# Performance work log

Measured on AMD Instinct MI355X. Metric: run time of the kernel, lower is better.

## Reference

```python
import jax, jax.numpy as jnp
import numpy as np
from jax import lax

EPS = 1e-8
ROOT_2 = 1.41421
STYLE_SIZE = 512
OUT_CH = 512
STYLE_SCALE = (2.0 / STYLE_SIZE) ** 0.5   # Weight_Scaling(style_size): equalized-LR sqrt(2/fan_in)
OUT_SCALE = (2.0 / (OUT_CH * 1 * 1)) ** 0.5  # Weight_Scaling(out_channels*1*1)


def setup_inputs() -> dict:
    key = jax.random.key(0)
    ks = jax.random.split(key, 10)
    B, Cin, Cout, H, S = 8, 512, 512, 32, 512
    return {
        "x": jax.random.normal(ks[0], (B, Cin, H, H), dtype=jnp.float32),
        "style_base": jax.random.normal(ks[1], (B, S), dtype=jnp.float32),
        "noise": jax.random.normal(ks[2], (B, 1, 2 * H, 2 * H), dtype=jnp.float32),
        "t": jax.random.normal(ks[3], (B, Cout, 2 * H, 2 * H), dtype=jnp.float32),
        # learned params
        "affine_w": jax.random.normal(ks[4], (Cin, S), dtype=jnp.float32) * (1.0 / np.sqrt(S)),
        "affine_b": jnp.zeros((Cin,), dtype=jnp.float32),
        "conv_w": jax.random.normal(ks[5], (Cout, Cin, 3, 3), dtype=jnp.float32),
        "conv_b": jnp.zeros((1, Cout, 1, 1), dtype=jnp.float32),
        "prelu_a": jnp.asarray(0.25, dtype=jnp.float32),
        "noise_scalar": jnp.zeros((1, Cout, 1, 1), dtype=jnp.float32) + 0.1,
        "out_w": jax.random.normal(ks[6], (3, Cout, 1, 1), dtype=jnp.float32) * (1.0 / np.sqrt(Cout)),
        "out_b": jnp.zeros((3,), dtype=jnp.float32),
    }


def reference(x, style_base, noise, t, affine_w, affine_b, conv_w, conv_b,
              prelu_a, noise_scalar, out_w, out_b):
    B, Cin, H, W = x.shape
    # style_std = affine(Weight_Scaling(style_base)) + 1  -> [B, Cin]
    style_std = (style_base * STYLE_SCALE) @ affine_w.T + affine_b + 1.0

    # bilinear x2 upsample (align_corners=False == half-pixel, matches jax.image.resize)
    x = jax.image.resize(x, (B, Cin, 2 * H, 2 * W), method="bilinear")

    # modulated conv with L2 demodulation, expressed as input-scale + conv + output-scale
    # per-sample weight w_b[o,i,k,l] = w[o,i,k,l]*s[b,i] / ||w*s||_b,o
    wsq = jnp.sum(conv_w ** 2, axis=(2, 3))                      # [O, I]
    demod = 1.0 / jnp.sqrt(jnp.einsum("oi,bi->bo", wsq, style_std ** 2) + EPS)  # [B, O]
    xm = x * style_std[:, :, None, None]
    y = lax.conv_general_dilated(xm, conv_w, (1, 1), "SAME",
                                 dimension_numbers=("NCHW", "OIHW", "NCHW"))
    y = y * demod[:, :, None, None] + conv_b + noise_scalar * noise
    # PReLU (single shared slope)
    y = jnp.where(y >= 0, y, prelu_a * y)

    # out branch: skip add, scale, toRGB 1x1 conv, clamp
    y = (y + t) / ROOT_2
    out = lax.conv_general_dilated(y * OUT_SCALE, out_w, (1, 1), "SAME",
                                   dimension_numbers=("NCHW", "OIHW", "NCHW"))
    out = jnp.clip(out + out_b[None, :, None, None], 0.0, 1.0)
    return (y, out)
```

## Files before the change

### kernel.cpp

```cpp
#include <hip/hip_runtime.h>


typedef short bf16x8 __attribute__((ext_vector_type(8)));
typedef short short8v __attribute__((ext_vector_type(8)));
typedef float f32x16 __attribute__((ext_vector_type(16)));

#define WS_STYLE 0
#define WS_DEMOD 16384
#define WS_WSQ   32768
#define WS_WPACK 1081344
#define WS_XM    5799936

__device__ __forceinline__ short f2bf(float f) {
  unsigned u = __float_as_uint(f);
  u += 0x7FFFu + ((u >> 16) & 1u);
  return (short)(u >> 16);
}

__device__ __forceinline__ void gld16(const short* g, char* l) {
  __builtin_amdgcn_global_load_lds((const __attribute__((address_space(1))) void*)g,
                                   (__attribute__((address_space(3))) void*)l,
                                   16, 0, 0);
}

__global__ void k_style(const float* __restrict__ sb, const float* __restrict__ aw,
                        const float* __restrict__ ab, float* __restrict__ style) {
  __shared__ float s_sb[512];
  int b = blockIdx.x;
  for (int i = threadIdx.x; i < 512; i += 256) s_sb[i] = sb[b * 512 + i] * 0.0625f;
  __syncthreads();
  for (int i = threadIdx.x; i < 512; i += 256) {
    const float4* wrow = (const float4*)(aw + (size_t)i * 512);
    float acc = 0.f;
    #pragma unroll 4
    for (int s4 = 0; s4 < 128; ++s4) {
      float4 w4 = wrow[s4];
      float4 sv = *(const float4*)(s_sb + s4 * 4);
      acc += w4.x * sv.x + w4.y * sv.y + w4.z * sv.z + w4.w * sv.w;
    }
    style[b * 512 + i] = acc + ab[i] + 1.0f;
  }
}

__global__ void k_wsq(const float* __restrict__ cw, float* __restrict__ wsq) {
  int idx = blockIdx.x * 256 + threadIdx.x;
  const float* p = cw + (size_t)idx * 9;
  float s = 0.f;
  #pragma unroll
  for (int j = 0; j < 9; ++j) s += p[j] * p[j];
  wsq[idx] = s;
}

__global__ void k_demod(const float* __restrict__ wsq, const float* __restrict__ style,
                        float* __restrict__ demod) {
  int wid = threadIdx.x >> 6, lane = threadIdx.x & 63;
  int idx = blockIdx.x * 4 + wid;
  int b = idx >> 9, o = idx & 511;
  const float* wr = wsq + (size_t)o * 512;
  const float* ss = style + b * 512;
  float sum = 0.f;
  #pragma unroll
  for (int k = 0; k < 8; ++k) {
    int i = k * 64 + lane;
    float s = ss[i];
    sum += wr[i] * s * s;
  }
  #pragma unroll
  for (int off = 32; off; off >>= 1) sum += __shfl_down(sum, off);
  if (lane == 0) demod[b * 512 + o] = rsqrtf(sum + 1e-8f);
}

__global__ void k_upsample(const float* __restrict__ x, const float* __restrict__ style,
                           short* __restrict__ xm) {
  int b = blockIdx.x / 66, hp = blockIdx.x % 66;
  short* xmp = xm + ((size_t)b * 66 + hp) * 66 * 512;
  if (hp == 0 || hp == 65) {
    short8v z = {0, 0, 0, 0, 0, 0, 0, 0};
    for (int u = threadIdx.x; u < 66 * 512 / 8; u += 256) ((short8v*)xmp)[u] = z;
    return;
  }
  int h = hp - 1;
  int j0 = (h >> 1) - 1 + (h & 1);
  float fj = (h & 1) ? 0.25f : 0.75f;
  int j0c = j0 < 0 ? 0 : j0;
  int j1c = j0 + 1 > 31 ? 31 : j0 + 1;
  __shared__ float xt[2][64][33];
  int ccc = threadIdx.x & 63;
  int wsub = threadIdx.x >> 6;
  for (int c0 = 0; c0 < 512; c0 += 64) {
    __syncthreads();
    #pragma unroll 4
    for (int k = 0; k < 16; ++k) {
      int idx = k * 256 + threadIdx.x;
      int ii = idx & 31, cc = (idx >> 5) & 63, jj = idx >> 11;
      xt[jj][cc][ii] = x[(((size_t)b * 512 + c0 + cc) * 32 + (jj ? j1c : j0c)) * 32 + ii];
    }
    __syncthreads();
    float sstyle = style[b * 512 + c0 + ccc];
    #pragma unroll 4
    for (int wk = 0; wk < 16; ++wk) {
      int w = wk * 4 + wsub;
      int i0 = (w >> 1) - 1 + (w & 1);
      float fi = (w & 1) ? 0.25f : 0.75f;
      int i0c = i0 < 0 ? 0 : i0;
      int i1c = i0 + 1 > 31 ? 31 : i0 + 1;
      float v0 = xt[0][ccc][i0c] * (1.f - fi) + xt[0][ccc][i1c] * fi;
      float v1 = xt[1][ccc][i0c] * (1.f - fi) + xt[1][ccc][i1c] * fi;
      float v = (v0 * (1.f - fj) + v1 * fj) * sstyle;
      xmp[(size_t)(w + 1) * 512 + c0 + ccc] = f2bf(v);
    }
    if (wsub == 0) {
      xmp[c0 + ccc] = 0;
      xmp[(size_t)65 * 512 + c0 + ccc] = 0;
    }
  }
}

__global__ void k_packw(const float* __restrict__ cw, short* __restrict__ wpk) {
  int unit = blockIdx.x * 256 + threadIdx.x;
  int s = unit >> 11;
  int rem = unit & 2047;
  int o = rem >> 2, sp = rem & 3;
  int tap = s >> 4, cc = s & 15;
  int i0 = cc * 32 + ((sp ^ (o & 3)) << 3);
  const float* src = cw + ((size_t)o * 512 + i0) * 9 + tap;
  short8v v;
  #pragma unroll
  for (int j = 0; j < 8; ++j) v[j] = f2bf(src[j * 9]);
  *(short8v*)(wpk + (size_t)unit * 8) = v;
}

__global__ __launch_bounds__(512, 2) void k_conv(
    const short* __restrict__ xm, const short* __restrict__ wpk,
    const float* __restrict__ demod, const float* __restrict__ convb,
    const float* __restrict__ nscal, const float* __restrict__ noise,
    const float* __restrict__ t, const float* __restrict__ prelu_a,
    float* __restrict__ y) {
  __shared__ char XMs[2][25344];
  __shared__ char WTs[2][16384];

  int tid = threadIdx.x;
  int bid = blockIdx.x;
  int nt = bid & 1, sp_t = bid >> 1;
  int b = sp_t >> 4, hq = sp_t & 15;
  int wid = tid >> 6, lane = tid & 63;
  int wo = wid & 1, wsrow = wid >> 1;
  int l31 = lane & 31, lg = lane >> 5;

  const short* xb = xm + ((size_t)b * 66 + hq * 4) * 66 * 512;
  int wb0 = ((wo * 128 + l31) << 6) + ((lg ^ (l31 & 3)) << 4);

  #pragma unroll
  for (int k = 0; k < 3; ++k) {
    int u = k * 512 + tid;
    int r = u / 264, rem = u - r * 264;
    int wp = rem >> 2, spp = rem & 3;
    gld16(xb + (size_t)(r * 66 + wp) * 512 + ((spp ^ (wp & 3)) << 3), XMs[0] + u * 16);
  }
  if (tid < 48) {
    int u = 1536 + tid;
    int rem = u - 1320;
    int wp = rem >> 2, spp = rem & 3;
    gld16(xb + (size_t)(5 * 66 + wp) * 512 + ((spp ^ (wp & 3)) << 3), XMs[0] + u * 16);
  }
  {
    const short* wsrc = wpk + (size_t)(nt * 256) * 32;
    gld16(wsrc + tid * 8, WTs[0] + tid * 16);
    gld16(wsrc + (512 + tid) * 8, WTs[0] + (512 + tid) * 16);
  }

  f32x16 zf = {0,0,0,0,0,0,0,0,0,0,0,0,0,0,0,0};
  f32x16 acc[4][2];
  #pragma unroll
  for (int i = 0; i < 4; ++i) { acc[i][0] = zf; acc[i][1] = zf; }

  __syncthreads();

  #pragma unroll 1
  for (int cc = 0; cc < 16; ++cc) {
    const char* XMc = XMs[cc & 1];
    char* XMn = XMs[(cc & 1) ^ 1];
    int pw = cc & 1;
    #pragma unroll
    for (int tap = 0; tap < 9; ++tap) {
      const int kh = tap / 3, kw = tap % 3;
      const char* WTc = WTs[(pw + tap) & 1];
      char* WTn = (char*)WTs[(pw + tap + 1) & 1];

      if (!(cc == 15 && tap == 8)) {
        int ntap = (tap < 8) ? (tap + 1) : 0;
        int ncc  = (tap < 8) ? cc : (cc + 1);
        const short* wsrc = wpk + ((size_t)((ntap * 16 + ncc) * 512) + nt * 256) * 32;
        gld16(wsrc + tid * 8, WTn + tid * 16);
        gld16(wsrc + (512 + tid) * 8, WTn + (512 + tid) * 16);
      }
      if (tap >= 3 && cc < 15) {
        const int r = tap - 3;
        if (tid < 264) {
          int wp = tid >> 2, spp = tid & 3;
          gld16(xb + (size_t)(r * 66 + wp) * 512 + (cc + 1) * 32 + ((spp ^ (wp & 3)) << 3),
                XMn + (r * 264 + tid) * 16);
        }
      }

      int a = l31 + kw;
      int xo = ((wsrow + kh) * 66 + a) * 64 + ((lg ^ (a & 3)) << 4);
      bf16x8 xf00 = *(const bf16x8*)(XMc + xo);
      bf16x8 xf01 = *(const bf16x8*)(XMc + xo + 2048);
      bf16x8 xf10 = *(const bf16x8*)(XMc + (xo ^ 32));
      bf16x8 xf11 = *(const bf16x8*)(XMc + ((xo ^ 32) + 2048));
      bf16x8 wf00 = *(const bf16x8*)(WTc + wb0);
      bf16x8 wf01 = *(const bf16x8*)(WTc + wb0 + 2048);
      bf16x8 wf02 = *(const bf16x8*)(WTc + wb0 + 4096);
      bf16x8 wf03 = *(const bf16x8*)(WTc + wb0 + 6144);
      bf16x8 wf10 = *(const bf16x8*)(WTc + (wb0 ^ 32));
      bf16x8 wf11 = *(const bf16x8*)(WTc + ((wb0 ^ 32) + 2048));
      bf16x8 wf12 = *(const bf16x8*)(WTc + ((wb0 ^ 32) + 4096));
      bf16x8 wf13 = *(const bf16x8*)(WTc + ((wb0 ^ 32) + 6144));

      acc[0][0] = __builtin_amdgcn_mfma_f32_32x32x16_bf16(wf00, xf00, acc[0][0], 0, 0, 0);
      acc[0][1] = __builtin_amdgcn_mfma_f32_32x32x16_bf16(wf00, xf01, acc[0][1], 0, 0, 0);
      acc[1][0] = __builtin_amdgcn_mfma_f32_32x32x16_bf16(wf01, xf00, acc[1][0], 0, 0, 0);
      acc[1][1] = __builtin_amdgcn_mfma_f32_32x32x16_bf16(wf01, xf01, acc[1][1], 0, 0, 0);
      acc[2][0] = __builtin_amdgcn_mfma_f32_32x32x16_bf16(wf02, xf00, acc[2][0], 0, 0, 0);
      acc[2][1] = __builtin_amdgcn_mfma_f32_32x32x16_bf16(wf02, xf01, acc[2][1], 0, 0, 0);
      acc[3][0] = __builtin_amdgcn_mfma_f32_32x32x16_bf16(wf03, xf00, acc[3][0], 0, 0, 0);
      acc[3][1] = __builtin_amdgcn_mfma_f32_32x32x16_bf16(wf03, xf01, acc[3][1], 0, 0, 0);
      acc[0][0] = __builtin_amdgcn_mfma_f32_32x32x16_bf16(wf10, xf10, acc[0][0], 0, 0, 0);
      acc[0][1] = __builtin_amdgcn_mfma_f32_32x32x16_bf16(wf10, xf11, acc[0][1], 0, 0, 0);
      acc[1][0] = __builtin_amdgcn_mfma_f32_32x32x16_bf16(wf11, xf10, acc[1][0], 0, 0, 0);
      acc[1][1] = __builtin_amdgcn_mfma_f32_32x32x16_bf16(wf11, xf11, acc[1][1], 0, 0, 0);
      acc[2][0] = __builtin_amdgcn_mfma_f32_32x32x16_bf16(wf12, xf10, acc[2][0], 0, 0, 0);
      acc[2][1] = __builtin_amdgcn_mfma_f32_32x32x16_bf16(wf12, xf11, acc[2][1], 0, 0, 0);
      acc[3][0] = __builtin_amdgcn_mfma_f32_32x32x16_bf16(wf13, xf10, acc[3][0], 0, 0, 0);
      acc[3][1] = __builtin_amdgcn_mfma_f32_32x32x16_bf16(wf13, xf11, acc[3][1], 0, 0, 0);

      __syncthreads();
    }
  }

  float pa = prelu_a[0];
  const float inv_r2 = 1.0f / 1.41421f;
  int h = hq * 4 + wsrow;
  float nz0 = noise[((size_t)b * 64 + h) * 64 + l31];
  float nz1 = noise[((size_t)b * 64 + h) * 64 + 32 + l31];
  #pragma unroll
  for (int cf = 0; cf < 4; ++cf) {
    #pragma unroll
    for (int reg = 0; reg < 16; ++reg) {
      int orow = (reg & 3) + 8 * (reg >> 2) + 4 * lg;
      int o = nt * 256 + wo * 128 + cf * 32 + orow;
      float dm = demod[b * 512 + o];
      float cb = convb[o];
      float ns = nscal[o];
      #pragma unroll
      for (int nf = 0; nf < 2; ++nf) {
        int w = nf * 32 + l31;
        float v = acc[cf][nf][reg];
        v = v * dm + cb + ns * (nf ? nz1 : nz0);
        v = (v >= 0.f) ? v : pa * v;
        size_t oi = (((size_t)b * 512 + o) * 64 + h) * 64 + w;
        v = (v + t[oi]) * inv_r2;
        y[oi] = v;
      }
    }
  }
}

__global__ void k_rgb(const float* __restrict__ y, const float* __restrict__ ow,
                      const float* __restrict__ ob, float* __restrict__ out) {
  int b = blockIdx.x >> 6, h = blockIdx.x & 63;
  int w = threadIdx.x & 63, g = threadIdx.x >> 6;
  const float* yb = y + (((size_t)b * 512) * 64 + h) * 64 + w;
  float s0 = 0.f, s1 = 0.f, s2 = 0.f;
  for (int o = g * 128; o < g * 128 + 128; ++o) {
    float v = yb[(size_t)o * 4096];
    s0 += v * ow[o];
    s1 += v * ow[512 + o];
    s2 += v * ow[1024 + o];
  }
  __shared__ float red[3][4][64];
  red[0][g][w] = s0; red[1][g][w] = s1; red[2][g][w] = s2;
  __syncthreads();
  if (threadIdx.x < 192) {
    int c = threadIdx.x >> 6, ww = threadIdx.x & 63;
    float s = red[c][0][ww] + red[c][1][ww] + red[c][2][ww] + red[c][3][ww];
    s = s * 0.0625f + ob[c];
    s = fminf(fmaxf(s, 0.f), 1.f);
    out[(((size_t)b * 3 + c) * 64 + h) * 64 + ww] = s;
  }
}

extern "C" void kernel_launch(void* const* d_in, const int* in_sizes, int n_in,
                              void* d_out, int out_size, void* d_ws, size_t ws_size,
                              hipStream_t stream) {
  const float* x     = (const float*)d_in[0];
  const float* sb    = (const float*)d_in[1];
  const float* noise = (const float*)d_in[2];
  const float* t     = (const float*)d_in[3];
  const float* aw    = (const float*)d_in[4];
  const float* ab    = (const float*)d_in[5];
  const float* cw    = (const float*)d_in[6];
  const float* cb    = (const float*)d_in[7];
  const float* pa    = (const float*)d_in[8];
  const float* ns    = (const float*)d_in[9];
  const float* ow    = (const float*)d_in[10];
  const float* ob    = (const float*)d_in[11];
  char* ws = (char*)d_ws;
  float* style = (float*)(ws + WS_STYLE);
  float* demod = (float*)(ws + WS_DEMOD);
  float* wsq   = (float*)(ws + WS_WSQ);
  short* wpk   = (short*)(ws + WS_WPACK);
  short* xm    = (short*)(ws + WS_XM);
  float* y   = (float*)d_out;
  float* out = y + 16777216;

  k_style<<<8, 256, 0, stream>>>(sb, aw, ab, style);
  k_wsq<<<1024, 256, 0, stream>>>(cw, wsq);
  k_demod<<<1024, 256, 0, stream>>>(wsq, style, demod);
  k_upsample<<<528, 256, 0, stream>>>(x, style, xm);
  k_packw<<<1152, 256, 0, stream>>>(cw, wpk);
  k_conv<<<256, 512, 0, stream>>>(xm, wpk, demod, cb, ns, noise, t, pa, y);
  k_rgb<<<512, 256, 0, stream>>>(y, ow, ob, out);
}
```

Before: 269.9 us.

## Halve conv spatial tile to 2 rows, 256 threads, new LDS swizzle, MFMA priority

The conv kernel now computes 2 output rows per block with 4 waves instead of 4 rows with 8 waves, doubling the grid to 512 blocks. The aim is better CU occupancy and load balance across the many compute units. The LDS XOR swizzle changes from (idx&3) to ((idx>>1)&3), applied consistently in weight packing and activation loads, to reduce bank conflicts. The activation prefetch is spread over taps 0-5, and s_setprio raises wave priority around the MFMA block. In exchange, each weight tile is reused over half as many pixels, so weight traffic from L2 per FLOP doubles.

Result: faster. 254.2 us (-5.8%).

```diff
diff --git a/kernel.cpp b/kernel.cpp
--- a/kernel.cpp
+++ b/kernel.cpp
@@ -122,7 +122,7 @@
   int rem = unit & 2047;
   int o = rem >> 2, sp = rem & 3;
   int tap = s >> 4, cc = s & 15;
-  int i0 = cc * 32 + ((sp ^ (o & 3)) << 3);
+  int i0 = cc * 32 + ((sp ^ ((o >> 1) & 3)) << 3);
   const float* src = cw + ((size_t)o * 512 + i0) * 9 + tap;
   short8v v;
   #pragma unroll
@@ -130,43 +130,42 @@
   *(short8v*)(wpk + (size_t)unit * 8) = v;
 }
 
-__global__ __launch_bounds__(512, 2) void k_conv(
+__global__ __launch_bounds__(256, 2) void k_conv(
     const short* __restrict__ xm, const short* __restrict__ wpk,
     const float* __restrict__ demod, const float* __restrict__ convb,
     const float* __restrict__ nscal, const float* __restrict__ noise,
     const float* __restrict__ t, const float* __restrict__ prelu_a,
     float* __restrict__ y) {
-  __shared__ char XMs[2][25344];
+  __shared__ char XMs[2][16896];
   __shared__ char WTs[2][16384];
 
   int tid = threadIdx.x;
   int bid = blockIdx.x;
-  int nt = bid & 1, sp_t = bid >> 1;
-  int b = sp_t >> 4, hq = sp_t & 15;
+  int nt = bid & 1, hpair = (bid >> 1) & 31, b = bid >> 6;
   int wid = tid >> 6, lane = tid & 63;
   int wo = wid & 1, wsrow = wid >> 1;
   int l31 = lane & 31, lg = lane >> 5;
 
-  const short* xb = xm + ((size_t)b * 66 + hq * 4) * 66 * 512;
-  int wb0 = ((wo * 128 + l31) << 6) + ((lg ^ (l31 & 3)) << 4);
-
-  #pragma unroll
-  for (int k = 0; k < 3; ++k) {
-    int u = k * 512 + tid;
+  const short* xb = xm + ((size_t)b * 66 + hpair * 2) * 66 * 512;
+  int wb0 = ((wo * 128 + l31) << 6) + ((lg ^ ((l31 >> 1) & 3)) << 4);
+
+  #pragma unroll
+  for (int k = 0; k < 4; ++k) {
+    int u = k * 256 + tid;
     int r = u / 264, rem = u - r * 264;
     int wp = rem >> 2, spp = rem & 3;
-    gld16(xb + (size_t)(r * 66 + wp) * 512 + ((spp ^ (wp & 3)) << 3), XMs[0] + u * 16);
-  }
-  if (tid < 48) {
-    int u = 1536 + tid;
-    int rem = u - 1320;
+    gld16(xb + (size_t)(r * 66 + wp) * 512 + ((spp ^ ((wp >> 1) & 3)) << 3), XMs[0] + u * 16);
+  }
+  if (tid < 32) {
+    int u = 1024 + tid;
+    int rem = u - 792;
     int wp = rem >> 2, spp = rem & 3;
-    gld16(xb + (size_t)(5 * 66 + wp) * 512 + ((spp ^ (wp & 3)) << 3), XMs[0] + u * 16);
-  }
-  {
-    const short* wsrc = wpk + (size_t)(nt * 256) * 32;
-    gld16(wsrc + tid * 8, WTs[0] + tid * 16);
-    gld16(wsrc + (512 + tid) * 8, WTs[0] + (512 + tid) * 16);
+    gld16(xb + (size_t)(3 * 66 + wp) * 512 + ((spp ^ ((wp >> 1) & 3)) << 3), XMs[0] + u * 16);
+  }
+  #pragma unroll
+  for (int k = 0; k < 4; ++k) {
+    int u = k * 256 + tid;
+    gld16(wpk + (size_t)(nt * 256) * 32 + u * 8, WTs[0] + u * 16);
   }
 
   f32x16 zf = {0,0,0,0,0,0,0,0,0,0,0,0,0,0,0,0};
@@ -180,31 +179,32 @@
   for (int cc = 0; cc < 16; ++cc) {
     const char* XMc = XMs[cc & 1];
     char* XMn = XMs[(cc & 1) ^ 1];
-    int pw = cc & 1;
     #pragma unroll
     for (int tap = 0; tap < 9; ++tap) {
       const int kh = tap / 3, kw = tap % 3;
-      const char* WTc = WTs[(pw + tap) & 1];
-      char* WTn = (char*)WTs[(pw + tap + 1) & 1];
+      const char* WTc = WTs[(cc + tap) & 1];
+      char* WTn = (char*)WTs[(cc + tap + 1) & 1];
 
       if (!(cc == 15 && tap == 8)) {
         int ntap = (tap < 8) ? (tap + 1) : 0;
         int ncc  = (tap < 8) ? cc : (cc + 1);
         const short* wsrc = wpk + ((size_t)((ntap * 16 + ncc) * 512) + nt * 256) * 32;
-        gld16(wsrc + tid * 8, WTn + tid * 16);
-        gld16(wsrc + (512 + tid) * 8, WTn + (512 + tid) * 16);
-      }
-      if (tap >= 3 && cc < 15) {
-        const int r = tap - 3;
-        if (tid < 264) {
-          int wp = tid >> 2, spp = tid & 3;
-          gld16(xb + (size_t)(r * 66 + wp) * 512 + (cc + 1) * 32 + ((spp ^ (wp & 3)) << 3),
-                XMn + (r * 264 + tid) * 16);
+        #pragma unroll
+        for (int k = 0; k < 4; ++k) {
+          int u = k * 256 + tid;
+          gld16(wsrc + u * 8, WTn + u * 16);
         }
       }
+      if (tap <= 5 && cc < 15 && tid < 176) {
+        int u = tap * 176 + tid;
+        int r = u / 264, rem = u - r * 264;
+        int wp = rem >> 2, spp = rem & 3;
+        gld16(xb + (size_t)(r * 66 + wp) * 512 + (cc + 1) * 32 + ((spp ^ ((wp >> 1) & 3)) << 3),
+              XMn + u * 16);
+      }
 
       int a = l31 + kw;
-      int xo = ((wsrow + kh) * 66 + a) * 64 + ((lg ^ (a & 3)) << 4);
+      int xo = ((wsrow + kh) * 66 + a) * 64 + ((lg ^ ((a >> 1) & 3)) << 4);
       bf16x8 xf00 = *(const bf16x8*)(XMc + xo);
       bf16x8 xf01 = *(const bf16x8*)(XMc + xo + 2048);
       bf16x8 xf10 = *(const bf16x8*)(XMc + (xo ^ 32));
@@ -218,6 +218,7 @@
       bf16x8 wf12 = *(const bf16x8*)(WTc + ((wb0 ^ 32) + 4096));
       bf16x8 wf13 = *(const bf16x8*)(WTc + ((wb0 ^ 32) + 6144));
 
+      __builtin_amdgcn_s_setprio(1);
       acc[0][0] = __builtin_amdgcn_mfma_f32_32x32x16_bf16(wf00, xf00, acc[0][0], 0, 0, 0);
       acc[0][1] = __builtin_amdgcn_mfma_f32_32x32x16_bf16(wf00, xf01, acc[0][1], 0, 0, 0);
       acc[1][0] = __builtin_amdgcn_mfma_f32_32x32x16_bf16(wf01, xf00, acc[1][0], 0, 0, 0);
@@ -234,6 +235,7 @@
       acc[2][1] = __builtin_amdgcn_mfma_f32_32x32x16_bf16(wf12, xf11, acc[2][1], 0, 0, 0);
       acc[3][0] = __builtin_amdgcn_mfma_f32_32x32x16_bf16(wf13, xf10, acc[3][0], 0, 0, 0);
       acc[3][1] = __builtin_amdgcn_mfma_f32_32x32x16_bf16(wf13, xf11, acc[3][1], 0, 0, 0);
+      __builtin_amdgcn_s_setprio(0);
 
       __syncthreads();
     }
@@ -241,7 +243,7 @@
 
   float pa = prelu_a[0];
   const float inv_r2 = 1.0f / 1.41421f;
-  int h = hq * 4 + wsrow;
+  int h = hpair * 2 + wsrow;
   float nz0 = noise[((size_t)b * 64 + h) * 64 + l31];
   float nz1 = noise[((size_t)b * 64 + h) * 64 + 32 + l31];
   #pragma unroll
@@ -320,6 +322,6 @@
   k_demod<<<1024, 256, 0, stream>>>(wsq, style, demod);
   k_upsample<<<528, 256, 0, stream>>>(x, style, xm);
   k_packw<<<1152, 256, 0, stream>>>(cw, wpk);
-  k_conv<<<256, 512, 0, stream>>>(xm, wpk, demod, cb, ns, noise, t, pa, y);
+  k_conv<<<512, 256, 0, stream>>>(xm, wpk, demod, cb, ns, noise, t, pa, y);
   k_rgb<<<512, 256, 0, stream>>>(y, ow, ob, out);
 }
```
